# Kernel optimization log

Hardware: AMD Instinct MI355X
Metric: run time of the kernel (lower is better)

## Reference

```python
import jax, jax.numpy as jnp
import numpy as np

NB = 5  # frequency bands


def _ln(x, g, b, eps=1e-5):
    m = jnp.mean(x, axis=-1, keepdims=True)
    v = jnp.var(x, axis=-1, keepdims=True)
    return (x - m) / jnp.sqrt(v + eps) * g + b


def _graph_adj(x, adj_w, sw1, sb1, sw2, sb2, pos_factor, pos_enc):
    # x: [B, D, N] -> degree-normalized adjacency [B, N, N]
    d = x.shape[1]
    xt = jnp.swapaxes(x, 1, 2)  # [B, N, D]
    # concat-MLP first layer split: cat(xi, xj) @ W1 == xi @ W1[:d] + xj @ W1[d:]
    a = xt @ sw1[:d]
    bpart = xt @ sw1[d:]
    h = jax.nn.elu(a[:, :, None, :] + bpart[:, None, :, :] + sb1)  # [B, N, N, H]
    dyn = jax.nn.sigmoid(jnp.squeeze(h @ sw2, -1) + sb2)  # [B, N, N]
    static = jax.nn.softmax(adj_w, axis=-1)
    pos = jax.nn.softmax(pos_enc, axis=-1)
    comb = jax.nn.softmax(static + dyn + pos_factor * pos, axis=-1)
    deg = jnp.sum(comb, axis=-1)
    dis = (deg + 1e-8) ** -0.5
    return dis[:, :, None] * comb * dis[:, None, :]


def _gcn(x, adj, w, b):
    # x: [B, D, N], adj: [B, N, N] -> [B, D_out, N]
    xt = jnp.swapaxes(x, 1, 2)
    out = jnp.einsum('bij,bjd->bid', adj, xt) @ w + b
    return jnp.swapaxes(out, 1, 2)


def _mha(x, qkv_w, qkv_b, ow, ob, nh=4):
    B, S, D = x.shape
    dh = D // nh
    q, k, v = jnp.split(x @ qkv_w + qkv_b, 3, axis=-1)
    q = q.reshape(B, S, nh, dh)
    k = k.reshape(B, S, nh, dh)
    v = v.reshape(B, S, nh, dh)
    att = jax.nn.softmax(jnp.einsum('bihd,bjhd->bhij', q, k) / float(np.sqrt(dh)), axis=-1)
    o = jnp.einsum('bhij,bjhd->bihd', att, v).reshape(B, S, D)
    return o @ ow + ob


def setup_inputs():
    key = jax.random.key(0)
    B, D, N = 16, 256, 64
    ks = iter(jax.random.split(key, 40))

    def rn(shape, s=0.05):
        return jax.random.normal(next(ks), shape, dtype=jnp.float32) * s

    eyeN = jnp.eye(N, dtype=jnp.float32)
    return dict(
        feature=jax.random.normal(next(ks), (B, NB * D, 1, N), dtype=jnp.float32),
        l_adj_w=jnp.tile(eyeN[None], (NB, 1, 1)),
        l_sim_w1=rn((NB, 2 * D, D)), l_sim_b1=jnp.zeros((NB, D), jnp.float32),
        l_sim_w2=rn((NB, D, 1)), l_sim_b2=jnp.zeros((NB, 1), jnp.float32),
        l_pos_factor=jnp.full((NB,), 0.5, jnp.float32),
        l_pos_enc=jnp.tile(eyeN[None], (NB, 1, 1)),
        l_gcn_w=rn((NB, D, D)), l_gcn_b=jnp.zeros((NB, D), jnp.float32),
        g_adj_w=jnp.eye(NB, dtype=jnp.float32),
        g_sim_w1=rn((2 * D, D)), g_sim_b1=jnp.zeros((D,), jnp.float32),
        g_sim_w2=rn((D, 1)), g_sim_b2=jnp.zeros((1,), jnp.float32),
        g_pos_factor=jnp.float32(0.5),
        g_pos_enc=jnp.eye(NB, dtype=jnp.float32),
        g_gcn_w=rn((D, D)), g_gcn_b=jnp.zeros((D,), jnp.float32),
        qkv_w=rn((D, 3 * D)), qkv_b=jnp.zeros((3 * D,), jnp.float32),
        attn_ow=rn((D, D)), attn_ob=jnp.zeros((D,), jnp.float32),
        ln1_g=jnp.ones((D,), jnp.float32), ln1_b=jnp.zeros((D,), jnp.float32),
        ln2_g=jnp.ones((D,), jnp.float32), ln2_b=jnp.zeros((D,), jnp.float32),
        mlp_w1=rn((D, 4 * D)), mlp_b1=jnp.zeros((4 * D,), jnp.float32),
        mlp_w2=rn((4 * D, D)), mlp_b2=jnp.zeros((D,), jnp.float32),
        imp_w=rn((NB, N, 1)), imp_b=jnp.zeros((NB, 1), jnp.float32),
    )


def reference(feature, l_adj_w, l_sim_w1, l_sim_b1, l_sim_w2, l_sim_b2,
              l_pos_factor, l_pos_enc, l_gcn_w, l_gcn_b,
              g_adj_w, g_sim_w1, g_sim_b1, g_sim_w2, g_sim_b2,
              g_pos_factor, g_pos_enc, g_gcn_w, g_gcn_b,
              qkv_w, qkv_b, attn_ow, attn_ob,
              ln1_g, ln1_b, ln2_g, ln2_b,
              mlp_w1, mlp_b1, mlp_w2, mlp_b2,
              imp_w, imp_b):
    B = feature.shape[0]
    D = l_gcn_w.shape[-1]
    N = feature.shape[-1]
    # [B, 5*D, 1, N] -> [5, B, D, N] band-major
    x5 = jnp.moveaxis(feature.reshape(B, NB, D, N), 1, 0)
    # per-band local graphs + GCNs (vmapped over the 5 bands)
    local_adj = jax.vmap(_graph_adj)(x5, l_adj_w, l_sim_w1, l_sim_b1,
                                     l_sim_w2, l_sim_b2, l_pos_factor, l_pos_enc)
    local_out = jax.vmap(_gcn)(x5, local_adj, l_gcn_w, l_gcn_b)  # [5, B, D, N]
    scale_nodes = jnp.moveaxis(jnp.mean(local_out, axis=-1), 0, 1)  # [B, 5, D]
    # cross-band attention block (pre: MHA + residual + LN, then MLP + residual + LN)
    attn = _mha(scale_nodes, qkv_w, qkv_b, attn_ow, attn_ob)
    h1 = _ln(scale_nodes + attn, ln1_g, ln1_b)
    mlp = jax.nn.gelu(h1 @ mlp_w1 + mlp_b1, approximate=False) @ mlp_w2 + mlp_b2
    se = _ln(h1 + mlp, ln2_g, ln2_b)  # [B, 5, D]
    # global scale graph over the 5 band nodes
    xg = jnp.swapaxes(se, 1, 2)  # [B, D, 5]
    g_adj = _graph_adj(xg, g_adj_w, g_sim_w1, g_sim_b1, g_sim_w2, g_sim_b2,
                       g_pos_factor, g_pos_enc)
    g_out = jnp.swapaxes(_gcn(xg, g_adj, g_gcn_w, g_gcn_b), 1, 2)  # [B, 5, D]
    # modulate each local band feature by its global scale vector
    enh = local_out * jnp.moveaxis(g_out, 1, 0)[..., None]  # [5, B, D, N]
    # per-band importance projection over channels: [5, B, D, 1]
    out5 = jnp.einsum('kbdn,kno->kbdo', enh, imp_w) + imp_b[:, None, None, :]
    output = jnp.moveaxis(out5, 0, 1).reshape(B, NB * D, 1, 1)
    return output, g_adj, jnp.moveaxis(local_out, 0, 1)
```

## Files before the change

kernel.cpp:

```cpp
#include <hip/hip_runtime.h>
#include <hip/hip_bf16.h>

#define NBANDS 5
#define BATCH  16
#define DIM    256
#define NNODE  64
#define SEQ    5

typedef __hip_bfloat16 bf16;
typedef unsigned short ushort_t;
typedef __attribute__((ext_vector_type(8))) short short8;
typedef __attribute__((ext_vector_type(4))) float float4v;

#define MFMA __builtin_amdgcn_mfma_f32_16x16x32_bf16

__device__ __forceinline__ float bu2f(ushort_t u){
    bf16 h = *reinterpret_cast<bf16*>(&u);
    return __bfloat162float(h);
}
__device__ __forceinline__ ushort_t f2bu(float x){
    bf16 h = __float2bfloat16(x);
    return *reinterpret_cast<ushort_t*>(&h);
}
__device__ __forceinline__ float elu(float v){
    return (v > 0.f) ? v : (__expf(v) - 1.f);
}

__global__ void __launch_bounds__(256) k_head(
    const float* __restrict__ l_adj_w, const float* __restrict__ l_pos_enc,
    const float* __restrict__ l_pf,
    const float* __restrict__ g_adj_w, const float* __restrict__ g_pos_enc,
    const float* __restrict__ g_pf,
    float* __restrict__ sbase, float* __restrict__ gbase,
    const float* __restrict__ w1, const float* __restrict__ gw,
    ushort_t* __restrict__ w1bt, ushort_t* __restrict__ gwbt)
{
    int blk = blockIdx.x;
    int tid = threadIdx.x;
    __shared__ ushort_t tile[64][65];

    if (blk < 80) {
        int r = blk*4 + (tid>>6);
        int k = r >> 6, i = r & 63;
        int t = tid & 63;
        float aw = l_adj_w[(k*NNODE + i)*NNODE + t];
        float pe = l_pos_enc[(k*NNODE + i)*NNODE + t];
        float m1 = aw, m2 = pe;
        for (int o=32;o>0;o>>=1){ m1 = fmaxf(m1, __shfl_xor(m1,o,64)); m2 = fmaxf(m2, __shfl_xor(m2,o,64)); }
        float e1 = __expf(aw-m1), e2 = __expf(pe-m2);
        float s1=e1, s2=e2;
        for (int o=32;o>0;o>>=1){ s1 += __shfl_xor(s1,o,64); s2 += __shfl_xor(s2,o,64); }
        float pf = l_pf[k];
        sbase[(k*NNODE+i)*NNODE + t] = e1/s1 + pf*(e2/s2);
    } else if (blk == 80) {
        if (tid < NBANDS) {
            int i = tid;
            float r1[NBANDS], r2[NBANDS];
            float m1=-1e30f, m2=-1e30f;
            for (int j=0;j<NBANDS;j++){
                r1[j]=g_adj_w[i*NBANDS+j]; r2[j]=g_pos_enc[i*NBANDS+j];
                m1=fmaxf(m1,r1[j]); m2=fmaxf(m2,r2[j]);
            }
            float s1=0.f,s2=0.f;
            for (int j=0;j<NBANDS;j++){ r1[j]=__expf(r1[j]-m1); r2[j]=__expf(r2[j]-m2); s1+=r1[j]; s2+=r2[j]; }
            float pf = g_pf[0];
            for (int j=0;j<NBANDS;j++) gbase[i*NBANDS+j] = r1[j]/s1 + pf*(r2[j]/s2);
        }
    } else {
        int idx = blk - 81;
        int inst = idx >> 4;
        int t = idx & 15;
        int r0 = (t>>2)*64, c0 = (t&3)*64;
        const float* src; ushort_t* dst;
        if (inst < 10){
            int k = inst>>1, half = inst&1;
            src = w1  + ((size_t)k*512 + half*256)*256;
            dst = w1bt+ ((size_t)k*512 + half*256)*256;
        } else {
            int k = inst-10;
            src = gw  + (size_t)k*65536;
            dst = gwbt+ (size_t)k*65536;
        }
        int jj = tid & 63, i4 = tid >> 6;
        for (int p=0;p<16;p++){
            int i = p*4 + i4;
            tile[i][jj] = f2bu(src[(size_t)(r0+i)*256 + c0 + jj]);
        }
        __syncthreads();
        for (int p=0;p<16;p++){
            int i = p*4 + i4;
            dst[(size_t)(c0+i)*256 + r0 + jj] = tile[jj][i];
        }
    }
}

__global__ void __launch_bounds__(512) k_graph(
    const float* __restrict__ feat,
    const ushort_t* __restrict__ w1bt, const float* __restrict__ b1,
    const float* __restrict__ w2, const float* __restrict__ b2arr,
    const float* __restrict__ sbase,
    const ushort_t* __restrict__ gwbt, const float* __restrict__ gb,
    const float* __restrict__ imp_w,
    float* __restrict__ out_local,
    float* __restrict__ scalew4, float* __restrict__ impw4)
{
    int kb = blockIdx.x % 80;
    int iq = blockIdx.x / 80;
    int k  = kb >> 4;
    int b  = kb & 15;
    int i0 = iq << 4;
    int tid = threadIdx.x;
    int w = tid >> 6, lane = tid & 63, c16 = lane & 15, quad = lane >> 4;

    __shared__ ushort_t Ubuf[64*266 + 8];
    __shared__ ushort_t as[16][264];
    __shared__ ushort_t cs[16][72];
    __shared__ ushort_t ys[16][264];
    __shared__ float w2s[DIM];

    const float* src = feat + ((size_t)b*NBANDS + k)*DIM*NNODE;

    int il0 = w*2, il1 = w*2 + 1;
    float sb0 = sbase[(k*NNODE + i0 + il0)*NNODE + lane];
    float sb1 = sbase[(k*NNODE + i0 + il1)*NNODE + lane];
    float sbias2 = b2arr[k];

    if (tid < DIM) w2s[tid] = w2[k*DIM + tid];
    #pragma unroll
    for (int u = 0; u < 32; ++u){
        int idx = u*512 + tid;
        Ubuf[(idx & 63)*264 + (idx >> 6)] = f2bu(src[idx]);
    }
    __syncthreads();

    int col0 = w*32 + c16;
    int col1 = col0 + 16;

    const ushort_t* Ba = w1bt + (size_t)k*512*DIM;
    const ushort_t* Bb = Ba + 256*DIM;
    float4v z = {0.f,0.f,0.f,0.f};
    float4v aA0=z, aA1=z;
    float4v aB00=z,aB01=z,aB10=z,aB11=z,aB20=z,aB21=z,aB30=z,aB31=z;
    #pragma unroll
    for (int ks = 0; ks < 8; ++ks){
        int ko = ks*32 + quad*8;
        short8 fa = *reinterpret_cast<const short8*>(&Ubuf[(i0 + c16)*264 + ko]);
        short8 f0 = *reinterpret_cast<const short8*>(&Ubuf[( 0 + c16)*264 + ko]);
        short8 f1 = *reinterpret_cast<const short8*>(&Ubuf[(16 + c16)*264 + ko]);
        short8 f2 = *reinterpret_cast<const short8*>(&Ubuf[(32 + c16)*264 + ko]);
        short8 f3 = *reinterpret_cast<const short8*>(&Ubuf[(48 + c16)*264 + ko]);
        short8 wa0 = *reinterpret_cast<const short8*>(Ba + (size_t)col0*DIM + ko);
        short8 wa1 = *reinterpret_cast<const short8*>(Ba + (size_t)col1*DIM + ko);
        short8 wb0 = *reinterpret_cast<const short8*>(Bb + (size_t)col0*DIM + ko);
        short8 wb1 = *reinterpret_cast<const short8*>(Bb + (size_t)col1*DIM + ko);
        aA0  = MFMA(fa, wa0, aA0, 0,0,0);
        aA1  = MFMA(fa, wa1, aA1, 0,0,0);
        aB00 = MFMA(f0, wb0, aB00, 0,0,0);
        aB01 = MFMA(f0, wb1, aB01, 0,0,0);
        aB10 = MFMA(f1, wb0, aB10, 0,0,0);
        aB11 = MFMA(f1, wb1, aB11, 0,0,0);
        aB20 = MFMA(f2, wb0, aB20, 0,0,0);
        aB21 = MFMA(f2, wb1, aB21, 0,0,0);
        aB30 = MFMA(f3, wb0, aB30, 0,0,0);
        aB31 = MFMA(f3, wb1, aB31, 0,0,0);
    }
    __syncthreads();
    {
        float bias0 = b1[k*DIM + col0];
        float bias1 = b1[k*DIM + col1];
        int r0 = quad*4;
        #pragma unroll
        for (int r = 0; r < 4; ++r){
            as[r0 + r][col0] = f2bu(aA0[r] + bias0);
            as[r0 + r][col1] = f2bu(aA1[r] + bias1);
            Ubuf[( 0 + r0 + r)*266 + col0] = f2bu(aB00[r]);
            Ubuf[( 0 + r0 + r)*266 + col1] = f2bu(aB01[r]);
            Ubuf[(16 + r0 + r)*266 + col0] = f2bu(aB10[r]);
            Ubuf[(16 + r0 + r)*266 + col1] = f2bu(aB11[r]);
            Ubuf[(32 + r0 + r)*266 + col0] = f2bu(aB20[r]);
            Ubuf[(32 + r0 + r)*266 + col1] = f2bu(aB21[r]);
            Ubuf[(48 + r0 + r)*266 + col0] = f2bu(aB30[r]);
            Ubuf[(48 + r0 + r)*266 + col1] = f2bu(aB31[r]);
        }
    }
    __syncthreads();

    {
        const ushort_t* bd = Ubuf + 266*lane;
        const ushort_t* a0p = as[il0];
        const ushort_t* a1p = as[il1];
        float acc0 = 0.f, acc1 = 0.f;
        #pragma unroll 4
        for (int dd = 0; dd < 64; ++dd){
            unsigned int blo = *reinterpret_cast<const unsigned int*>(bd + dd*4);
            unsigned int bhi = *reinterpret_cast<const unsigned int*>(bd + dd*4 + 2);
            ushort4 a0 = *reinterpret_cast<const ushort4*>(a0p + dd*4);
            ushort4 a1 = *reinterpret_cast<const ushort4*>(a1p + dd*4);
            float4 wv  = *reinterpret_cast<const float4*>(&w2s[dd*4]);
            float bx = bu2f((ushort_t)(blo & 0xffffu));
            float by = bu2f((ushort_t)(blo >> 16));
            float bz = bu2f((ushort_t)(bhi & 0xffffu));
            float bq = bu2f((ushort_t)(bhi >> 16));
            acc0 += elu(bu2f(a0.x)+bx)*wv.x + elu(bu2f(a0.y)+by)*wv.y
                  + elu(bu2f(a0.z)+bz)*wv.z + elu(bu2f(a0.w)+bq)*wv.w;
            acc1 += elu(bu2f(a1.x)+bx)*wv.x + elu(bu2f(a1.y)+by)*wv.y
                  + elu(bu2f(a1.z)+bz)*wv.z + elu(bu2f(a1.w)+bq)*wv.w;
        }
        float sg0 = 1.f/(1.f + __expf(-(acc0 + sbias2)));
        float sg1 = 1.f/(1.f + __expf(-(acc1 + sbias2)));
        float val0 = sb0 + sg0;
        float val1 = sb1 + sg1;
        float m0 = val0, m1 = val1;
        for (int o=32;o>0;o>>=1){ m0 = fmaxf(m0, __shfl_xor(m0,o,64)); m1 = fmaxf(m1, __shfl_xor(m1,o,64)); }
        float e0 = __expf(val0 - m0), e1 = __expf(val1 - m1);
        float s0 = e0, s1 = e1;
        for (int o=32;o>0;o>>=1){ s0 += __shfl_xor(s0,o,64); s1 += __shfl_xor(s1,o,64); }
        cs[il0][lane] = f2bu(e0/s0);
        cs[il1][lane] = f2bu(e1/s1);
    }
    __syncthreads();

    float4v aY0 = z, aY1 = z;
    {
        #pragma unroll
        for (int ks = 0; ks < 2; ++ks){
            int ko = ks*32 + quad*8;
            short8 af = *reinterpret_cast<const short8*>(&cs[c16][ko]);
            const float* f0p = src + (size_t)col0*NNODE + ko;
            const float* f1p = src + (size_t)col1*NNODE + ko;
            float4 x0 = *reinterpret_cast<const float4*>(f0p);
            float4 x1 = *reinterpret_cast<const float4*>(f0p+4);
            float4 y0 = *reinterpret_cast<const float4*>(f1p);
            float4 y1 = *reinterpret_cast<const float4*>(f1p+4);
            short8 bf0, bf1;
            bf0[0]=(short)f2bu(x0.x); bf0[1]=(short)f2bu(x0.y); bf0[2]=(short)f2bu(x0.z); bf0[3]=(short)f2bu(x0.w);
            bf0[4]=(short)f2bu(x1.x); bf0[5]=(short)f2bu(x1.y); bf0[6]=(short)f2bu(x1.z); bf0[7]=(short)f2bu(x1.w);
            bf1[0]=(short)f2bu(y0.x); bf1[1]=(short)f2bu(y0.y); bf1[2]=(short)f2bu(y0.z); bf1[3]=(short)f2bu(y0.w);
            bf1[4]=(short)f2bu(y1.x); bf1[5]=(short)f2bu(y1.y); bf1[6]=(short)f2bu(y1.z); bf1[7]=(short)f2bu(y1.w);
            aY0 = MFMA(af, bf0, aY0, 0,0,0);
            aY1 = MFMA(af, bf1, aY1, 0,0,0);
        }
        #pragma unroll
        for (int r=0;r<4;++r){
            ys[quad*4 + r][col0] = f2bu(aY0[r]);
            ys[quad*4 + r][col1] = f2bu(aY1[r]);
        }
    }
    __syncthreads();

    {
        float4v aG0 = z, aG1 = z;
        const ushort_t* Bg = gwbt + (size_t)k*DIM*DIM;
        #pragma unroll
        for (int ks = 0; ks < 8; ++ks){
            int ko = ks*32 + quad*8;
            short8 af = *reinterpret_cast<const short8*>(&ys[c16][ko]);
            short8 g0 = *reinterpret_cast<const short8*>(Bg + (size_t)col0*DIM + ko);
            short8 g1 = *reinterpret_cast<const short8*>(Bg + (size_t)col1*DIM + ko);
            aG0 = MFMA(af, g0, aG0, 0,0,0);
            aG1 = MFMA(af, g1, aG1, 0,0,0);
        }
        int nb = i0 + quad*4;
        float iw0 = imp_w[k*NNODE + nb + 0];
        float iw1 = imp_w[k*NNODE + nb + 1];
        float iw2 = imp_w[k*NNODE + nb + 2];
        float iw3 = imp_w[k*NNODE + nb + 3];
        size_t obase = ((size_t)b*NBANDS + k)*DIM;

        float bias0 = gb[k*DIM + col0];
        float v0 = aG0[0]+bias0, v1 = aG0[1]+bias0, v2 = aG0[2]+bias0, v3 = aG0[3]+bias0;
        float4 vv = make_float4(v0,v1,v2,v3);
        *reinterpret_cast<float4*>(&out_local[(obase + col0)*NNODE + nb]) = vv;
        float s  = v0+v1+v2+v3;
        float di = v0*iw0 + v1*iw1 + v2*iw2 + v3*iw3;
        s  += __shfl_xor(s,16,64);  s  += __shfl_xor(s,32,64);
        di += __shfl_xor(di,16,64); di += __shfl_xor(di,32,64);
        if (quad == 0){
            size_t o = ((size_t)iq*80 + b*SEQ + k)*DIM + col0;
            scalew4[o] = s;
            impw4[o]   = di;
        }

        float bias1 = gb[k*DIM + col1];
        v0 = aG1[0]+bias1; v1 = aG1[1]+bias1; v2 = aG1[2]+bias1; v3 = aG1[3]+bias1;
        vv = make_float4(v0,v1,v2,v3);
        *reinterpret_cast<float4*>(&out_local[(obase + col1)*NNODE + nb]) = vv;
        s  = v0+v1+v2+v3;
        di = v0*iw0 + v1*iw1 + v2*iw2 + v3*iw3;
        s  += __shfl_xor(s,16,64);  s  += __shfl_xor(s,32,64);
        di += __shfl_xor(di,16,64); di += __shfl_xor(di,32,64);
        if (quad == 0){
            size_t o = ((size_t)iq*80 + b*SEQ + k)*DIM + col1;
            scalew4[o] = s;
            impw4[o]   = di;
        }
    }
}

__global__ void __launch_bounds__(256) k_qkv_gemv(const float* __restrict__ scalew4,
                        const float* __restrict__ w, const float* __restrict__ bias,
                        float* __restrict__ out)
{
    int row = blockIdx.x / 12;
    int n0 = (blockIdx.x % 12) * 64;
    int tid = threadIdx.x;
    int c = tid & 63, s = tid >> 6;
    __shared__ float xs[DIM];
    __shared__ float part[4][64];
    {
        size_t basei = (size_t)row*DIM + tid;
        xs[tid] = (scalew4[basei] + scalew4[20480 + basei]
                 + scalew4[40960 + basei] + scalew4[61440 + basei]) * (1.f/64.f);
    }
    __syncthreads();
    const float* wp = w + (size_t)(s*64)*768 + n0 + c;
    const float* xp = xs + s*64;
    float acc = 0.f;
    #pragma unroll 8
    for (int i = 0; i < 64; ++i) acc += xp[i] * wp[(size_t)i*768];
    part[s][c] = acc;
    __syncthreads();
    if (s == 0){
        out[(size_t)row*768 + n0 + c] = bias[n0+c] + part[0][c]+part[1][c]+part[2][c]+part[3][c];
    }
}

template<int COLS, int SLICES>
__global__ void __launch_bounds__(256) k_gemv(const float* __restrict__ x, const float* __restrict__ w,
                       const float* __restrict__ bias, float* __restrict__ out,
                       int K, int N, int act)
{
    int chunks = N / COLS;
    int row = blockIdx.x / chunks;
    int n0 = (blockIdx.x % chunks) * COLS;
    int c = threadIdx.x % COLS, s = threadIdx.x / COLS;
    __shared__ float xs[1024];
    __shared__ float part[SLICES][COLS];
    for (int i = threadIdx.x; i < K; i += 256) xs[i] = x[(size_t)row*K + i];
    __syncthreads();
    int klen = K / SLICES;
    const float* wp = w + (size_t)(s*klen)*N + n0 + c;
    const float* xp = xs + s*klen;
    float acc = 0.f;
    #pragma unroll 8
    for (int i = 0; i < klen; ++i) acc += xp[i] * wp[(size_t)i*N];
    part[s][c] = acc;
    __syncthreads();
    if (s == 0){
        float v = bias[n0+c];
        #pragma unroll
        for (int q=0;q<SLICES;q++) v += part[q][c];
        if (act) v = 0.5f*v*(1.f + erff(v*0.70710678118654752f));
        out[(size_t)row*N + n0 + c] = v;
    }
}

__global__ void __launch_bounds__(256) k_projattn(const float* __restrict__ qkvw,
                        const float* __restrict__ ow, const float* __restrict__ ob,
                        float* __restrict__ projw)
{
    int row = blockIdx.x / 4;
    int n0 = (blockIdx.x % 4) * 64;
    int b = row / SEQ, i = row % SEQ;
    int tid = threadIdx.x;
    int h = tid >> 6, l = tid & 63;
    __shared__ float xs[DIM];
    __shared__ float part[4][64];
    const float* base = qkvw + (size_t)b*SEQ*3*DIM;
    float qv = base[(size_t)i*3*DIM + h*64 + l];
    float pj[SEQ];
    #pragma unroll
    for (int j=0;j<SEQ;j++){
        float p = qv * base[(size_t)j*3*DIM + DIM + h*64 + l];
        for (int o=32;o>0;o>>=1) p += __shfl_xor(p,o,64);
        pj[j] = p * 0.125f;
    }
    float m = pj[0];
    #pragma unroll
    for (int j=1;j<SEQ;j++) m = fmaxf(m, pj[j]);
    float ssum = 0.f;
    #pragma unroll
    for (int j=0;j<SEQ;j++){ pj[j] = __expf(pj[j]-m); ssum += pj[j]; }
    float inv = 1.f/ssum;
    float o = 0.f;
    #pragma unroll
    for (int j=0;j<SEQ;j++) o += pj[j]*inv * base[(size_t)j*3*DIM + 2*DIM + h*64 + l];
    xs[tid] = o;
    __syncthreads();
    int c = tid & 63, s = tid >> 6;
    const float* wp = ow + (size_t)(s*64)*DIM + n0 + c;
    const float* xp = xs + s*64;
    float acc = 0.f;
    #pragma unroll 8
    for (int k=0;k<64;++k) acc += xp[k] * wp[(size_t)k*DIM];
    part[s][c] = acc;
    __syncthreads();
    if (s == 0){
        projw[(size_t)row*DIM + n0 + c] = ob[n0+c] + part[0][c]+part[1][c]+part[2][c]+part[3][c];
    }
}

__device__ __forceinline__ float block_ln(float v, int tid, float* red, float g, float bln)
{
    float s = v;
    for (int o=32;o>0;o>>=1) s += __shfl_xor(s,o,64);
    int wave = tid>>6, lane = tid&63;
    if (lane==0) red[wave] = s;
    __syncthreads();
    float mean = (red[0]+red[1]+red[2]+red[3]) * (1.f/DIM);
    float c = v - mean;
    float q = c*c;
    for (int o=32;o>0;o>>=1) q += __shfl_xor(q,o,64);
    __syncthreads();
    if (lane==0) red[wave] = q;
    __syncthreads();
    float var = (red[0]+red[1]+red[2]+red[3]) * (1.f/DIM);
    return c * rsqrtf(var + 1e-5f) * g + bln;
}

__global__ void __launch_bounds__(256) k_mlp1_ln(const float* __restrict__ projw,
                         const float* __restrict__ scalew4,
                         const float* __restrict__ ln1_g, const float* __restrict__ ln1_b,
                         const float* __restrict__ w1, const float* __restrict__ b1,
                         float* __restrict__ h1w, float* __restrict__ mhw)
{
    int row = blockIdx.x / 16;
    int n0 = (blockIdx.x % 16) * 64;
    int tid = threadIdx.x;
    __shared__ float xs[DIM];
    __shared__ float red[4];
    __shared__ float part[4][64];
    size_t basei = (size_t)row*DIM + tid;
    float sc = (scalew4[basei] + scalew4[20480 + basei]
              + scalew4[40960 + basei] + scalew4[61440 + basei]) * (1.f/64.f);
    float v = projw[basei] + sc;
    float h = block_ln(v, tid, red, ln1_g[tid], ln1_b[tid]);
    xs[tid] = h;
    if ((blockIdx.x % 16) == 0) h1w[basei] = h;
    __syncthreads();
    int c = tid & 63, s = tid >> 6;
    const float* wp = w1 + (size_t)(s*64)*1024 + n0 + c;
    const float* xp = xs + s*64;
    float acc = 0.f;
    #pragma unroll 8
    for (int i=0;i<64;++i) acc += xp[i] * wp[(size_t)i*1024];
    part[s][c] = acc;
    __syncthreads();
    if (s == 0){
        float o = b1[n0+c] + part[0][c] + part[1][c] + part[2][c] + part[3][c];
        o = 0.5f*o*(1.f + erff(o*0.70710678118654752f));
        mhw[(size_t)row*1024 + n0 + c] = o;
    }
}

__global__ void __launch_bounds__(256) k_gab_ln(const float* __restrict__ m2w,
                        const float* __restrict__ h1w,
                        const float* __restrict__ ln2_g, const float* __restrict__ ln2_b,
                        const float* __restrict__ gw1, const float* __restrict__ gb1,
                        float* __restrict__ sew, float* __restrict__ gaw, float* __restrict__ gbw)
{
    int row = blockIdx.x / 4;
    int n0 = (blockIdx.x % 4) * 64;
    int tid = threadIdx.x;
    __shared__ float xs[DIM];
    __shared__ float red[4];
    __shared__ float partA[4][64];
    __shared__ float partB[4][64];
    float v = m2w[(size_t)row*DIM + tid] + h1w[(size_t)row*DIM + tid];
    float h = block_ln(v, tid, red, ln2_g[tid], ln2_b[tid]);
    xs[tid] = h;
    if ((blockIdx.x % 4) == 0) sew[(size_t)row*DIM + tid] = h;
    __syncthreads();
    int c = tid & 63, s = tid >> 6;
    const float* wpA = gw1 + (size_t)(s*64)*DIM + n0 + c;
    const float* wpB = wpA + (size_t)DIM*DIM;
    const float* xp = xs + s*64;
    float aA = 0.f, aB = 0.f;
    #pragma unroll 8
    for (int i=0;i<64;++i){
        float xv = xp[i];
        aA += xv * wpA[(size_t)i*DIM];
        aB += xv * wpB[(size_t)i*DIM];
    }
    partA[s][c] = aA;
    partB[s][c] = aB;
    __syncthreads();
    if (s == 0){
        gaw[(size_t)row*DIM + n0 + c] = gb1[n0+c] + partA[0][c]+partA[1][c]+partA[2][c]+partA[3][c];
        gbw[(size_t)row*DIM + n0 + c] = partB[0][c]+partB[1][c]+partB[2][c]+partB[3][c];
    }
}

__global__ void __launch_bounds__(256) k_goutfin(const float* __restrict__ gaw,
                        const float* __restrict__ gbw,
                        const float* __restrict__ gw2, const float* __restrict__ gb2,
                        const float* __restrict__ gbase,
                        const float* __restrict__ sew,
                        const float* __restrict__ ggw, const float* __restrict__ ggb,
                        const float* __restrict__ impw4, const float* __restrict__ imp_b,
                        float* __restrict__ out0, float* __restrict__ out_gadj)
{
    int row = blockIdx.x / 4;
    int n0 = (blockIdx.x % 4) * 64;
    int b = row / SEQ, i = row % SEQ;
    int tid = threadIdx.x;
    int wave = tid >> 6, lane = tid & 63;
    __shared__ float dyn_s[SEQ];
    __shared__ float xs[DIM];
    __shared__ float part[4][64];
    for (int j = wave; j < SEQ; j += 4){
        const float* gar = gaw + (size_t)row*DIM;
        const float* gbr = gbw + ((size_t)b*SEQ + j)*DIM;
        float acc = 0.f;
        #pragma unroll
        for (int m=0;m<4;m++){
            int dd = lane + m*64;
            float v = gar[dd] + gbr[dd];
            acc += elu(v) * gw2[dd];
        }
        for (int o=32;o>0;o>>=1) acc += __shfl_xor(acc,o,64);
        if (lane==0) dyn_s[j] = acc;
    }
    __syncthreads();
    float gc[SEQ];
    {
        float sb2 = gb2[0];
        float m = -1e30f;
        #pragma unroll
        for (int j=0;j<SEQ;j++){
            float sg = 1.f/(1.f+__expf(-(dyn_s[j]+sb2)));
            gc[j] = gbase[i*SEQ+j] + sg;
            m = fmaxf(m, gc[j]);
        }
        float ssum=0.f;
        #pragma unroll
        for (int j=0;j<SEQ;j++){ gc[j]=__expf(gc[j]-m); ssum+=gc[j]; }
        float inv = 1.f/ssum;
        #pragma unroll
        for (int j=0;j<SEQ;j++) gc[j] *= inv;
    }
    if (n0 == 0 && tid < SEQ) out_gadj[((size_t)b*SEQ+i)*SEQ + tid] = gc[tid];
    float t = 0.f;
    #pragma unroll
    for (int j=0;j<SEQ;j++) t += gc[j]*sew[((size_t)b*SEQ + j)*DIM + tid];
    xs[tid] = t;
    __syncthreads();
    int c = tid & 63, s = tid >> 6;
    const float* wp = ggw + (size_t)(s*64)*DIM + n0 + c;
    const float* xp = xs + s*64;
    float acc = 0.f;
    #pragma unroll 8
    for (int k=0;k<64;++k) acc += xp[k] * wp[(size_t)k*DIM];
    part[s][c] = acc;
    __syncthreads();
    if (s == 0){
        float g = ggb[n0+c] + part[0][c]+part[1][c]+part[2][c]+part[3][c];
        size_t o = (size_t)row*DIM + n0 + c;
        float imps = impw4[o] + impw4[20480 + o] + impw4[40960 + o] + impw4[61440 + o];
        out0[o] = g * imps + imp_b[i];
    }
}

extern "C" void kernel_launch(void* const* d_in, const int* in_sizes, int n_in,
                              void* d_out, int out_size, void* d_ws, size_t ws_size,
                              hipStream_t stream)
{
    const float* feature      = (const float*)d_in[0];
    const float* l_adj_w      = (const float*)d_in[1];
    const float* l_sim_w1     = (const float*)d_in[2];
    const float* l_sim_b1     = (const float*)d_in[3];
    const float* l_sim_w2     = (const float*)d_in[4];
    const float* l_sim_b2     = (const float*)d_in[5];
    const float* l_pos_factor = (const float*)d_in[6];
    const float* l_pos_enc    = (const float*)d_in[7];
    const float* l_gcn_w      = (const float*)d_in[8];
    const float* l_gcn_b      = (const float*)d_in[9];
    const float* g_adj_w      = (const float*)d_in[10];
    const float* g_sim_w1     = (const float*)d_in[11];
    const float* g_sim_b1     = (const float*)d_in[12];
    const float* g_sim_w2     = (const float*)d_in[13];
    const float* g_sim_b2     = (const float*)d_in[14];
    const float* g_pos_factor = (const float*)d_in[15];
    const float* g_pos_enc    = (const float*)d_in[16];
    const float* g_gcn_w      = (const float*)d_in[17];
    const float* g_gcn_b      = (const float*)d_in[18];
    const float* qkv_w        = (const float*)d_in[19];
    const float* qkv_b        = (const float*)d_in[20];
    const float* attn_ow      = (const float*)d_in[21];
    const float* attn_ob      = (const float*)d_in[22];
    const float* ln1_g        = (const float*)d_in[23];
    const float* ln1_b        = (const float*)d_in[24];
    const float* ln2_g        = (const float*)d_in[25];
    const float* ln2_b        = (const float*)d_in[26];
    const float* mlp_w1       = (const float*)d_in[27];
    const float* mlp_b1       = (const float*)d_in[28];
    const float* mlp_w2       = (const float*)d_in[29];
    const float* mlp_b2       = (const float*)d_in[30];
    const float* imp_w        = (const float*)d_in[31];
    const float* imp_b        = (const float*)d_in[32];

    float* out0      = (float*)d_out;
    float* out_gadj  = out0 + (size_t)BATCH*NBANDS*DIM;
    float* out_local = out_gadj + (size_t)BATCH*NBANDS*NBANDS;

    ushort_t* w1bt = (ushort_t*)d_ws;
    ushort_t* gwbt = w1bt + (size_t)NBANDS*512*DIM;
    float* fp = (float*)(gwbt + (size_t)NBANDS*DIM*DIM);
    float* sbase   = fp; fp += NBANDS*NNODE*NNODE;
    float* gbase   = fp; fp += 32;
    float* scalew4 = fp; fp += 4*BATCH*SEQ*DIM;
    float* impw4   = fp; fp += 4*BATCH*SEQ*DIM;
    float* qkvw    = fp; fp += BATCH*SEQ*3*DIM;
    float* projw   = fp; fp += BATCH*SEQ*DIM;
    float* h1w     = fp; fp += BATCH*SEQ*DIM;
    float* mhw     = fp; fp += BATCH*SEQ*4*DIM;
    float* m2w     = fp; fp += BATCH*SEQ*DIM;
    float* sew     = fp; fp += BATCH*SEQ*DIM;
    float* gaw     = fp; fp += BATCH*SEQ*DIM;
    float* gbw     = fp; fp += BATCH*SEQ*DIM;

    const int ROWS = BATCH*SEQ;

    k_head<<<321, 256, 0, stream>>>(l_adj_w, l_pos_enc, l_pos_factor,
                                    g_adj_w, g_pos_enc, g_pos_factor,
                                    sbase, gbase,
                                    l_sim_w1, l_gcn_w, w1bt, gwbt);
    k_graph<<<NBANDS*BATCH*4, 512, 0, stream>>>(feature, w1bt, l_sim_b1,
                                    l_sim_w2, l_sim_b2, sbase,
                                    gwbt, l_gcn_b, imp_w,
                                    out_local, scalew4, impw4);
    k_qkv_gemv<<<ROWS*12, 256, 0, stream>>>(scalew4, qkv_w, qkv_b, qkvw);
    k_projattn<<<ROWS*4, 256, 0, stream>>>(qkvw, attn_ow, attn_ob, projw);
    k_mlp1_ln<<<ROWS*16, 256, 0, stream>>>(projw, scalew4, ln1_g, ln1_b, mlp_w1, mlp_b1, h1w, mhw);
    k_gemv<32,8><<<ROWS*8, 256, 0, stream>>>(mhw, mlp_w2, mlp_b2, m2w, 1024, 256, 0);
    k_gab_ln<<<ROWS*4, 256, 0, stream>>>(m2w, h1w, ln2_g, ln2_b, g_sim_w1, g_sim_b1, sew, gaw, gbw);
    k_goutfin<<<ROWS*4, 256, 0, stream>>>(gaw, gbw, g_sim_w2, g_sim_b2, gbase,
                                          sew, g_gcn_w, g_gcn_b, impw4, imp_b,
                                          out0, out_gadj);
}
```

Before: 215.8 us.

## Merge six tail kernels into one cooperative kernel with grid syncs

The six small GEMV/attention/LayerNorm tail kernels become a single cooperative kernel whose stages are separated by grid.sync() and use grid-stride loops over the original block tasks. The goal is to remove five kernel launch gaps and tail drains between tiny dependent stages. k_graph also changes: the feature transpose now packs 8 bf16 values per 16-byte LDS store, the w2 staging buffer is dropped in favour of direct global reads, and the ys buffer reuses Ubuf to cut shared-memory use. The risks are grid-sync overhead, and a launch failure if 960 blocks cannot all be co-resident for the cooperative launch.

After: 795.0 us. +268.3%, slower.

```diff
diff --git a/kernel.cpp b/kernel.cpp
--- a/kernel.cpp
+++ b/kernel.cpp
@@ -1,5 +1,8 @@
 #include <hip/hip_runtime.h>
 #include <hip/hip_bf16.h>
+#include <hip/hip_cooperative_groups.h>
+
+namespace cg = cooperative_groups;
 
 #define NBANDS 5
 #define BATCH  16
@@ -24,6 +27,9 @@
 }
 __device__ __forceinline__ float elu(float v){
     return (v > 0.f) ? v : (__expf(v) - 1.f);
+}
+__device__ __forceinline__ float sum4(const float* __restrict__ p, size_t i){
+    return p[i] + p[20480 + i] + p[40960 + i] + p[61440 + i];
 }
 
 __global__ void __launch_bounds__(256) k_head(
@@ -112,11 +118,10 @@
     int tid = threadIdx.x;
     int w = tid >> 6, lane = tid & 63, c16 = lane & 15, quad = lane >> 4;
 
-    __shared__ ushort_t Ubuf[64*266 + 8];
-    __shared__ ushort_t as[16][264];
-    __shared__ ushort_t cs[16][72];
-    __shared__ ushort_t ys[16][264];
-    __shared__ float w2s[DIM];
+    __shared__ __align__(16) ushort_t Ubuf[64*266 + 8];
+    __shared__ __align__(16) ushort_t as[16][260];
+    __shared__ __align__(16) ushort_t cs[16][72];
+    ushort_t* ys = Ubuf;
 
     const float* src = feat + ((size_t)b*NBANDS + k)*DIM*NNODE;
 
@@ -125,11 +130,15 @@
     float sb1 = sbase[(k*NNODE + i0 + il1)*NNODE + lane];
     float sbias2 = b2arr[k];
 
-    if (tid < DIM) w2s[tid] = w2[k*DIM + tid];
     #pragma unroll
-    for (int u = 0; u < 32; ++u){
-        int idx = u*512 + tid;
-        Ubuf[(idx & 63)*264 + (idx >> 6)] = f2bu(src[idx]);
+    for (int u = 0; u < 4; ++u){
+        int t = u*512 + tid;
+        int n = t & 63;
+        int d0 = (t >> 6) * 8;
+        short8 pk;
+        #pragma unroll
+        for (int i = 0; i < 8; ++i) pk[i] = (short)f2bu(src[(size_t)(d0+i)*NNODE + n]);
+        *reinterpret_cast<short8*>(&Ubuf[(size_t)n*264 + d0]) = pk;
     }
     __syncthreads();
 
@@ -187,8 +196,9 @@
 
     {
         const ushort_t* bd = Ubuf + 266*lane;
-        const ushort_t* a0p = as[il0];
-        const ushort_t* a1p = as[il1];
+        const ushort_t* a0p = &as[il0][0];
+        const ushort_t* a1p = &as[il1][0];
+        const float* w2p = w2 + k*DIM;
         float acc0 = 0.f, acc1 = 0.f;
         #pragma unroll 4
         for (int dd = 0; dd < 64; ++dd){
@@ -196,7 +206,7 @@
             unsigned int bhi = *reinterpret_cast<const unsigned int*>(bd + dd*4 + 2);
             ushort4 a0 = *reinterpret_cast<const ushort4*>(a0p + dd*4);
             ushort4 a1 = *reinterpret_cast<const ushort4*>(a1p + dd*4);
-            float4 wv  = *reinterpret_cast<const float4*>(&w2s[dd*4]);
+            float4 wv  = *reinterpret_cast<const float4*>(w2p + dd*4);
             float bx = bu2f((ushort_t)(blo & 0xffffu));
             float by = bu2f((ushort_t)(blo >> 16));
             float bz = bu2f((ushort_t)(bhi & 0xffffu));
@@ -220,8 +230,8 @@
     }
     __syncthreads();
 
-    float4v aY0 = z, aY1 = z;
     {
+        float4v aY0 = z, aY1 = z;
         #pragma unroll
         for (int ks = 0; ks < 2; ++ks){
             int ko = ks*32 + quad*8;
@@ -242,8 +252,8 @@
         }
         #pragma unroll
         for (int r=0;r<4;++r){
-            ys[quad*4 + r][col0] = f2bu(aY0[r]);
-            ys[quad*4 + r][col1] = f2bu(aY1[r]);
+            ys[(quad*4 + r)*264 + col0] = f2bu(aY0[r]);
+            ys[(quad*4 + r)*264 + col1] = f2bu(aY1[r]);
         }
     }
     __syncthreads();
@@ -254,7 +264,7 @@
         #pragma unroll
         for (int ks = 0; ks < 8; ++ks){
             int ko = ks*32 + quad*8;
-            short8 af = *reinterpret_cast<const short8*>(&ys[c16][ko]);
+            short8 af = *reinterpret_cast<const short8*>(&ys[c16*264 + ko]);
             short8 g0 = *reinterpret_cast<const short8*>(Bg + (size_t)col0*DIM + ko);
             short8 g1 = *reinterpret_cast<const short8*>(Bg + (size_t)col1*DIM + ko);
             aG0 = MFMA(af, g0, aG0, 0,0,0);
@@ -269,134 +279,31 @@
 
         float bias0 = gb[k*DIM + col0];
         float v0 = aG0[0]+bias0, v1 = aG0[1]+bias0, v2 = aG0[2]+bias0, v3 = aG0[3]+bias0;
-        float4 vv = make_float4(v0,v1,v2,v3);
-        *reinterpret_cast<float4*>(&out_local[(obase + col0)*NNODE + nb]) = vv;
+        *reinterpret_cast<float4*>(&out_local[(obase + col0)*NNODE + nb]) =
+            make_float4(v0,v1,v2,v3);
         float s  = v0+v1+v2+v3;
         float di = v0*iw0 + v1*iw1 + v2*iw2 + v3*iw3;
         s  += __shfl_xor(s,16,64);  s  += __shfl_xor(s,32,64);
         di += __shfl_xor(di,16,64); di += __shfl_xor(di,32,64);
         if (quad == 0){
-            size_t o = ((size_t)iq*80 + b*SEQ + k)*DIM + col0;
+            size_t o = (size_t)iq*20480 + ((size_t)b*SEQ + k)*DIM + col0;
             scalew4[o] = s;
             impw4[o]   = di;
         }
 
         float bias1 = gb[k*DIM + col1];
         v0 = aG1[0]+bias1; v1 = aG1[1]+bias1; v2 = aG1[2]+bias1; v3 = aG1[3]+bias1;
-        vv = make_float4(v0,v1,v2,v3);
-        *reinterpret_cast<float4*>(&out_local[(obase + col1)*NNODE + nb]) = vv;
+        *reinterpret_cast<float4*>(&out_local[(obase + col1)*NNODE + nb]) =
+            make_float4(v0,v1,v2,v3);
         s  = v0+v1+v2+v3;
         di = v0*iw0 + v1*iw1 + v2*iw2 + v3*iw3;
         s  += __shfl_xor(s,16,64);  s  += __shfl_xor(s,32,64);
         di += __shfl_xor(di,16,64); di += __shfl_xor(di,32,64);
         if (quad == 0){
-            size_t o = ((size_t)iq*80 + b*SEQ + k)*DIM + col1;
+            size_t o = (size_t)iq*20480 + ((size_t)b*SEQ + k)*DIM + col1;
             scalew4[o] = s;
             impw4[o]   = di;
         }
-    }
-}
-
-__global__ void __launch_bounds__(256) k_qkv_gemv(const float* __restrict__ scalew4,
-                        const float* __restrict__ w, const float* __restrict__ bias,
-                        float* __restrict__ out)
-{
-    int row = blockIdx.x / 12;
-    int n0 = (blockIdx.x % 12) * 64;
-    int tid = threadIdx.x;
-    int c = tid & 63, s = tid >> 6;
-    __shared__ float xs[DIM];
-    __shared__ float part[4][64];
-    {
-        size_t basei = (size_t)row*DIM + tid;
-        xs[tid] = (scalew4[basei] + scalew4[20480 + basei]
-                 + scalew4[40960 + basei] + scalew4[61440 + basei]) * (1.f/64.f);
-    }
-    __syncthreads();
-    const float* wp = w + (size_t)(s*64)*768 + n0 + c;
-    const float* xp = xs + s*64;
-    float acc = 0.f;
-    #pragma unroll 8
-    for (int i = 0; i < 64; ++i) acc += xp[i] * wp[(size_t)i*768];
-    part[s][c] = acc;
-    __syncthreads();
-    if (s == 0){
-        out[(size_t)row*768 + n0 + c] = bias[n0+c] + part[0][c]+part[1][c]+part[2][c]+part[3][c];
-    }
-}
-
-template<int COLS, int SLICES>
-__global__ void __launch_bounds__(256) k_gemv(const float* __restrict__ x, const float* __restrict__ w,
-                       const float* __restrict__ bias, float* __restrict__ out,
-                       int K, int N, int act)
-{
-    int chunks = N / COLS;
-    int row = blockIdx.x / chunks;
-    int n0 = (blockIdx.x % chunks) * COLS;
-    int c = threadIdx.x % COLS, s = threadIdx.x / COLS;
-    __shared__ float xs[1024];
-    __shared__ float part[SLICES][COLS];
-    for (int i = threadIdx.x; i < K; i += 256) xs[i] = x[(size_t)row*K + i];
-    __syncthreads();
-    int klen = K / SLICES;
-    const float* wp = w + (size_t)(s*klen)*N + n0 + c;
-    const float* xp = xs + s*klen;
-    float acc = 0.f;
-    #pragma unroll 8
-    for (int i = 0; i < klen; ++i) acc += xp[i] * wp[(size_t)i*N];
-    part[s][c] = acc;
-    __syncthreads();
-    if (s == 0){
-        float v = bias[n0+c];
-        #pragma unroll
-        for (int q=0;q<SLICES;q++) v += part[q][c];
-        if (act) v = 0.5f*v*(1.f + erff(v*0.70710678118654752f));
-        out[(size_t)row*N + n0 + c] = v;
-    }
-}
-
-__global__ void __launch_bounds__(256) k_projattn(const float* __restrict__ qkvw,
-                        const float* __restrict__ ow, const float* __restrict__ ob,
-                        float* __restrict__ projw)
-{
-    int row = blockIdx.x / 4;
-    int n0 = (blockIdx.x % 4) * 64;
-    int b = row / SEQ, i = row % SEQ;
-    int tid = threadIdx.x;
-    int h = tid >> 6, l = tid & 63;
-    __shared__ float xs[DIM];
-    __shared__ float part[4][64];
-    const float* base = qkvw + (size_t)b*SEQ*3*DIM;
-    float qv = base[(size_t)i*3*DIM + h*64 + l];
-    float pj[SEQ];
-    #pragma unroll
-    for (int j=0;j<SEQ;j++){
-        float p = qv * base[(size_t)j*3*DIM + DIM + h*64 + l];
-        for (int o=32;o>0;o>>=1) p += __shfl_xor(p,o,64);
-        pj[j] = p * 0.125f;
-    }
-    float m = pj[0];
-    #pragma unroll
-    for (int j=1;j<SEQ;j++) m = fmaxf(m, pj[j]);
-    float ssum = 0.f;
-    #pragma unroll
-    for (int j=0;j<SEQ;j++){ pj[j] = __expf(pj[j]-m); ssum += pj[j]; }
-    float inv = 1.f/ssum;
-    float o = 0.f;
-    #pragma unroll
-    for (int j=0;j<SEQ;j++) o += pj[j]*inv * base[(size_t)j*3*DIM + 2*DIM + h*64 + l];
-    xs[tid] = o;
-    __syncthreads();
-    int c = tid & 63, s = tid >> 6;
-    const float* wp = ow + (size_t)(s*64)*DIM + n0 + c;
-    const float* xp = xs + s*64;
-    float acc = 0.f;
-    #pragma unroll 8
-    for (int k=0;k<64;++k) acc += xp[k] * wp[(size_t)k*DIM];
-    part[s][c] = acc;
-    __syncthreads();
-    if (s == 0){
-        projw[(size_t)row*DIM + n0 + c] = ob[n0+c] + part[0][c]+part[1][c]+part[2][c]+part[3][c];
     }
 }
 
@@ -418,146 +325,220 @@
     return c * rsqrtf(var + 1e-5f) * g + bln;
 }
 
-__global__ void __launch_bounds__(256) k_mlp1_ln(const float* __restrict__ projw,
-                         const float* __restrict__ scalew4,
-                         const float* __restrict__ ln1_g, const float* __restrict__ ln1_b,
-                         const float* __restrict__ w1, const float* __restrict__ b1,
-                         float* __restrict__ h1w, float* __restrict__ mhw)
+struct TailArgs {
+    const float *scalew4, *impw4;
+    const float *qkv_w, *qkv_b, *attn_ow, *attn_ob;
+    const float *ln1_g, *ln1_b, *mlp_w1, *mlp_b1, *mlp_w2, *mlp_b2;
+    const float *ln2_g, *ln2_b, *gw1, *gb1, *gw2, *gb2, *gbase;
+    const float *ggw, *ggb, *imp_b;
+    float *qkvw, *projw, *h1w, *mhw, *m2w, *sew, *gaw, *gbw;
+    float *out0, *out_gadj;
+};
+
+__global__ void __launch_bounds__(256, 4) k_tail_coop(TailArgs A)
 {
-    int row = blockIdx.x / 16;
-    int n0 = (blockIdx.x % 16) * 64;
-    int tid = threadIdx.x;
-    __shared__ float xs[DIM];
-    __shared__ float red[4];
-    __shared__ float part[4][64];
-    size_t basei = (size_t)row*DIM + tid;
-    float sc = (scalew4[basei] + scalew4[20480 + basei]
-              + scalew4[40960 + basei] + scalew4[61440 + basei]) * (1.f/64.f);
-    float v = projw[basei] + sc;
-    float h = block_ln(v, tid, red, ln1_g[tid], ln1_b[tid]);
-    xs[tid] = h;
-    if ((blockIdx.x % 16) == 0) h1w[basei] = h;
-    __syncthreads();
-    int c = tid & 63, s = tid >> 6;
-    const float* wp = w1 + (size_t)(s*64)*1024 + n0 + c;
-    const float* xp = xs + s*64;
-    float acc = 0.f;
-    #pragma unroll 8
-    for (int i=0;i<64;++i) acc += xp[i] * wp[(size_t)i*1024];
-    part[s][c] = acc;
-    __syncthreads();
-    if (s == 0){
-        float o = b1[n0+c] + part[0][c] + part[1][c] + part[2][c] + part[3][c];
-        o = 0.5f*o*(1.f + erff(o*0.70710678118654752f));
-        mhw[(size_t)row*1024 + n0 + c] = o;
-    }
-}
-
-__global__ void __launch_bounds__(256) k_gab_ln(const float* __restrict__ m2w,
-                        const float* __restrict__ h1w,
-                        const float* __restrict__ ln2_g, const float* __restrict__ ln2_b,
-                        const float* __restrict__ gw1, const float* __restrict__ gb1,
-                        float* __restrict__ sew, float* __restrict__ gaw, float* __restrict__ gbw)
-{
-    int row = blockIdx.x / 4;
-    int n0 = (blockIdx.x % 4) * 64;
-    int tid = threadIdx.x;
-    __shared__ float xs[DIM];
-    __shared__ float red[4];
-    __shared__ float partA[4][64];
-    __shared__ float partB[4][64];
-    float v = m2w[(size_t)row*DIM + tid] + h1w[(size_t)row*DIM + tid];
-    float h = block_ln(v, tid, red, ln2_g[tid], ln2_b[tid]);
-    xs[tid] = h;
-    if ((blockIdx.x % 4) == 0) sew[(size_t)row*DIM + tid] = h;
-    __syncthreads();
-    int c = tid & 63, s = tid >> 6;
-    const float* wpA = gw1 + (size_t)(s*64)*DIM + n0 + c;
-    const float* wpB = wpA + (size_t)DIM*DIM;
-    const float* xp = xs + s*64;
-    float aA = 0.f, aB = 0.f;
-    #pragma unroll 8
-    for (int i=0;i<64;++i){
-        float xv = xp[i];
-        aA += xv * wpA[(size_t)i*DIM];
-        aB += xv * wpB[(size_t)i*DIM];
-    }
-    partA[s][c] = aA;
-    partB[s][c] = aB;
-    __syncthreads();
-    if (s == 0){
-        gaw[(size_t)row*DIM + n0 + c] = gb1[n0+c] + partA[0][c]+partA[1][c]+partA[2][c]+partA[3][c];
-        gbw[(size_t)row*DIM + n0 + c] = partB[0][c]+partB[1][c]+partB[2][c]+partB[3][c];
-    }
-}
-
-__global__ void __launch_bounds__(256) k_goutfin(const float* __restrict__ gaw,
-                        const float* __restrict__ gbw,
-                        const float* __restrict__ gw2, const float* __restrict__ gb2,
-                        const float* __restrict__ gbase,
-                        const float* __restrict__ sew,
-                        const float* __restrict__ ggw, const float* __restrict__ ggb,
-                        const float* __restrict__ impw4, const float* __restrict__ imp_b,
-                        float* __restrict__ out0, float* __restrict__ out_gadj)
-{
-    int row = blockIdx.x / 4;
-    int n0 = (blockIdx.x % 4) * 64;
-    int b = row / SEQ, i = row % SEQ;
+    cg::grid_group grid = cg::this_grid();
+    const int NBLK = gridDim.x;
     int tid = threadIdx.x;
     int wave = tid >> 6, lane = tid & 63;
-    __shared__ float dyn_s[SEQ];
-    __shared__ float xs[DIM];
-    __shared__ float part[4][64];
-    for (int j = wave; j < SEQ; j += 4){
-        const float* gar = gaw + (size_t)row*DIM;
-        const float* gbr = gbw + ((size_t)b*SEQ + j)*DIM;
+    __shared__ float xs[1024];
+    __shared__ float red[4];
+    __shared__ float part8[8][64];
+    __shared__ float dyn_s[8];
+
+    for (int t = blockIdx.x; t < 960; t += NBLK){
+        int row = t / 12, n0 = (t % 12) * 64;
+        int c = tid & 63, s = tid >> 6;
+        xs[tid] = sum4(A.scalew4, (size_t)row*DIM + tid) * (1.f/64.f);
+        __syncthreads();
+        const float* wp = A.qkv_w + (size_t)(s*64)*768 + n0 + c;
+        const float* xp = xs + s*64;
         float acc = 0.f;
-        #pragma unroll
-        for (int m=0;m<4;m++){
-            int dd = lane + m*64;
-            float v = gar[dd] + gbr[dd];
-            acc += elu(v) * gw2[dd];
-        }
-        for (int o=32;o>0;o>>=1) acc += __shfl_xor(acc,o,64);
-        if (lane==0) dyn_s[j] = acc;
-    }
-    __syncthreads();
-    float gc[SEQ];
-    {
-        float sb2 = gb2[0];
-        float m = -1e30f;
+        #pragma unroll 8
+        for (int i = 0; i < 64; ++i) acc += xp[i] * wp[(size_t)i*768];
+        part8[s][c] = acc;
+        __syncthreads();
+        if (s == 0)
+            A.qkvw[(size_t)row*768 + n0 + c] = A.qkv_b[n0+c]
+                + part8[0][c]+part8[1][c]+part8[2][c]+part8[3][c];
+        __syncthreads();
+    }
+    grid.sync();
+
+    for (int t = blockIdx.x; t < 320; t += NBLK){
+        int row = t / 4, n0 = (t % 4) * 64;
+        int b = row / SEQ, i = row % SEQ;
+        int h = wave, l = lane;
+        const float* base = A.qkvw + (size_t)b*SEQ*3*DIM;
+        float qv = base[(size_t)i*3*DIM + h*64 + l];
+        float pj[SEQ];
         #pragma unroll
         for (int j=0;j<SEQ;j++){
-            float sg = 1.f/(1.f+__expf(-(dyn_s[j]+sb2)));
-            gc[j] = gbase[i*SEQ+j] + sg;
-            m = fmaxf(m, gc[j]);
-        }
-        float ssum=0.f;
-        #pragma unroll
-        for (int j=0;j<SEQ;j++){ gc[j]=__expf(gc[j]-m); ssum+=gc[j]; }
+            float p = qv * base[(size_t)j*3*DIM + DIM + h*64 + l];
+            for (int o=32;o>0;o>>=1) p += __shfl_xor(p,o,64);
+            pj[j] = p * 0.125f;
+        }
+        float m = pj[0];
+        #pragma unroll
+        for (int j=1;j<SEQ;j++) m = fmaxf(m, pj[j]);
+        float ssum = 0.f;
+        #pragma unroll
+        for (int j=0;j<SEQ;j++){ pj[j] = __expf(pj[j]-m); ssum += pj[j]; }
         float inv = 1.f/ssum;
-        #pragma unroll
-        for (int j=0;j<SEQ;j++) gc[j] *= inv;
-    }
-    if (n0 == 0 && tid < SEQ) out_gadj[((size_t)b*SEQ+i)*SEQ + tid] = gc[tid];
-    float t = 0.f;
-    #pragma unroll
-    for (int j=0;j<SEQ;j++) t += gc[j]*sew[((size_t)b*SEQ + j)*DIM + tid];
-    xs[tid] = t;
-    __syncthreads();
-    int c = tid & 63, s = tid >> 6;
-    const float* wp = ggw + (size_t)(s*64)*DIM + n0 + c;
-    const float* xp = xs + s*64;
-    float acc = 0.f;
-    #pragma unroll 8
-    for (int k=0;k<64;++k) acc += xp[k] * wp[(size_t)k*DIM];
-    part[s][c] = acc;
-    __syncthreads();
-    if (s == 0){
-        float g = ggb[n0+c] + part[0][c]+part[1][c]+part[2][c]+part[3][c];
-        size_t o = (size_t)row*DIM + n0 + c;
-        float imps = impw4[o] + impw4[20480 + o] + impw4[40960 + o] + impw4[61440 + o];
-        out0[o] = g * imps + imp_b[i];
+        float o = 0.f;
+        #pragma unroll
+        for (int j=0;j<SEQ;j++) o += pj[j]*inv * base[(size_t)j*3*DIM + 2*DIM + h*64 + l];
+        xs[tid] = o;
+        __syncthreads();
+        int c = tid & 63, s = tid >> 6;
+        const float* wp = A.attn_ow + (size_t)(s*64)*DIM + n0 + c;
+        const float* xp = xs + s*64;
+        float acc = 0.f;
+        #pragma unroll 8
+        for (int kk=0;kk<64;++kk) acc += xp[kk] * wp[(size_t)kk*DIM];
+        part8[s][c] = acc;
+        __syncthreads();
+        if (s == 0)
+            A.projw[(size_t)row*DIM + n0 + c] = A.attn_ob[n0+c]
+                + part8[0][c]+part8[1][c]+part8[2][c]+part8[3][c];
+        __syncthreads();
+    }
+    grid.sync();
+
+    for (int t = blockIdx.x; t < 1280; t += NBLK){
+        int row = t / 16, n0 = (t % 16) * 64;
+        size_t basei = (size_t)row*DIM + tid;
+        float sc = sum4(A.scalew4, basei) * (1.f/64.f);
+        float v = A.projw[basei] + sc;
+        float hh = block_ln(v, tid, red, A.ln1_g[tid], A.ln1_b[tid]);
+        xs[tid] = hh;
+        if ((t % 16) == 0) A.h1w[basei] = hh;
+        __syncthreads();
+        int c = tid & 63, s = tid >> 6;
+        const float* wp = A.mlp_w1 + (size_t)(s*64)*1024 + n0 + c;
+        const float* xp = xs + s*64;
+        float acc = 0.f;
+        #pragma unroll 8
+        for (int i=0;i<64;++i) acc += xp[i] * wp[(size_t)i*1024];
+        part8[s][c] = acc;
+        __syncthreads();
+        if (s == 0){
+            float o = A.mlp_b1[n0+c] + part8[0][c]+part8[1][c]+part8[2][c]+part8[3][c];
+            o = 0.5f*o*(1.f + erff(o*0.70710678118654752f));
+            A.mhw[(size_t)row*1024 + n0 + c] = o;
+        }
+        __syncthreads();
+    }
+    grid.sync();
+
+    for (int t = blockIdx.x; t < 640; t += NBLK){
+        int row = t / 8, n0 = (t % 8) * 32;
+        for (int i = tid; i < 1024; i += 256) xs[i] = A.mhw[(size_t)row*1024 + i];
+        __syncthreads();
+        int c = tid & 31, s = tid >> 5;
+        const float* wp = A.mlp_w2 + (size_t)(s*128)*DIM + n0 + c;
+        const float* xp = xs + s*128;
+        float acc = 0.f;
+        #pragma unroll 8
+        for (int i = 0; i < 128; ++i) acc += xp[i] * wp[(size_t)i*DIM];
+        (&part8[0][0])[s*32 + c] = acc;
+        __syncthreads();
+        if (s == 0){
+            float v = A.mlp_b2[n0+c];
+            #pragma unroll
+            for (int q=0;q<8;q++) v += (&part8[0][0])[q*32 + c];
+            A.m2w[(size_t)row*DIM + n0 + c] = v;
+        }
+        __syncthreads();
+    }
+    grid.sync();
+
+    for (int t = blockIdx.x; t < 320; t += NBLK){
+        int row = t / 4, n0 = (t % 4) * 64;
+        float v = A.m2w[(size_t)row*DIM + tid] + A.h1w[(size_t)row*DIM + tid];
+        float hh = block_ln(v, tid, red, A.ln2_g[tid], A.ln2_b[tid]);
+        xs[tid] = hh;
+        if ((t % 4) == 0) A.sew[(size_t)row*DIM + tid] = hh;
+        __syncthreads();
+        int c = tid & 63, s = tid >> 6;
+        const float* wpA = A.gw1 + (size_t)(s*64)*DIM + n0 + c;
+        const float* wpB = wpA + (size_t)DIM*DIM;
+        const float* xp = xs + s*64;
+        float aA = 0.f, aB = 0.f;
+        #pragma unroll 8
+        for (int i=0;i<64;++i){
+            float xv = xp[i];
+            aA += xv * wpA[(size_t)i*DIM];
+            aB += xv * wpB[(size_t)i*DIM];
+        }
+        part8[s][c] = aA;
+        part8[4+s][c] = aB;
+        __syncthreads();
+        if (s == 0){
+            A.gaw[(size_t)row*DIM + n0 + c] = A.gb1[n0+c]
+                + part8[0][c]+part8[1][c]+part8[2][c]+part8[3][c];
+            A.gbw[(size_t)row*DIM + n0 + c] =
+                  part8[4][c]+part8[5][c]+part8[6][c]+part8[7][c];
+        }
+        __syncthreads();
+    }
+    grid.sync();
+
+    for (int t = blockIdx.x; t < 320; t += NBLK){
+        int row = t / 4, n0 = (t % 4) * 64;
+        int b = row / SEQ, i = row % SEQ;
+        for (int j = wave; j < SEQ; j += 4){
+            const float* gar = A.gaw + (size_t)row*DIM;
+            const float* gbr = A.gbw + ((size_t)b*SEQ + j)*DIM;
+            float acc = 0.f;
+            #pragma unroll
+            for (int m=0;m<4;m++){
+                int dd = lane + m*64;
+                float v = gar[dd] + gbr[dd];
+                acc += elu(v) * A.gw2[dd];
+            }
+            for (int o=32;o>0;o>>=1) acc += __shfl_xor(acc,o,64);
+            if (lane==0) dyn_s[j] = acc;
+        }
+        __syncthreads();
+        float gc[SEQ];
+        {
+            float sb2 = A.gb2[0];
+            float m = -1e30f;
+            #pragma unroll
+            for (int j=0;j<SEQ;j++){
+                float sg = 1.f/(1.f+__expf(-(dyn_s[j]+sb2)));
+                gc[j] = A.gbase[i*SEQ+j] + sg;
+                m = fmaxf(m, gc[j]);
+            }
+            float ssum=0.f;
+            #pragma unroll
+            for (int j=0;j<SEQ;j++){ gc[j]=__expf(gc[j]-m); ssum+=gc[j]; }
+            float inv = 1.f/ssum;
+            #pragma unroll
+            for (int j=0;j<SEQ;j++) gc[j] *= inv;
+        }
+        if (n0 == 0 && tid < SEQ) A.out_gadj[((size_t)b*SEQ+i)*SEQ + tid] = gc[tid];
+        float tv = 0.f;
+        #pragma unroll
+        for (int j=0;j<SEQ;j++) tv += gc[j]*A.sew[((size_t)b*SEQ + j)*DIM + tid];
+        xs[tid] = tv;
+        __syncthreads();
+        int c = tid & 63, s = tid >> 6;
+        const float* wp = A.ggw + (size_t)(s*64)*DIM + n0 + c;
+        const float* xp = xs + s*64;
+        float acc = 0.f;
+        #pragma unroll 8
+        for (int kk=0;kk<64;++kk) acc += xp[kk] * wp[(size_t)kk*DIM];
+        part8[s][c] = acc;
+        __syncthreads();
+        if (s == 0){
+            float g = A.ggb[n0+c] + part8[0][c]+part8[1][c]+part8[2][c]+part8[3][c];
+            size_t o = (size_t)row*DIM + n0 + c;
+            float imps = sum4(A.impw4, o);
+            A.out0[o] = g * imps + A.imp_b[i];
+        }
+        __syncthreads();
     }
 }
 
@@ -619,8 +600,6 @@
     float* gaw     = fp; fp += BATCH*SEQ*DIM;
     float* gbw     = fp; fp += BATCH*SEQ*DIM;
 
-    const int ROWS = BATCH*SEQ;
-
     k_head<<<321, 256, 0, stream>>>(l_adj_w, l_pos_enc, l_pos_factor,
                                     g_adj_w, g_pos_enc, g_pos_factor,
                                     sbase, gbase,
@@ -629,12 +608,25 @@
                                     l_sim_w2, l_sim_b2, sbase,
                                     gwbt, l_gcn_b, imp_w,
                                     out_local, scalew4, impw4);
-    k_qkv_gemv<<<ROWS*12, 256, 0, stream>>>(scalew4, qkv_w, qkv_b, qkvw);
-    k_projattn<<<ROWS*4, 256, 0, stream>>>(qkvw, attn_ow, attn_ob, projw);
-    k_mlp1_ln<<<ROWS*16, 256, 0, stream>>>(projw, scalew4, ln1_g, ln1_b, mlp_w1, mlp_b1, h1w, mhw);
-    k_gemv<32,8><<<ROWS*8, 256, 0, stream>>>(mhw, mlp_w2, mlp_b2, m2w, 1024, 256, 0);
-    k_gab_ln<<<ROWS*4, 256, 0, stream>>>(m2w, h1w, ln2_g, ln2_b, g_sim_w1, g_sim_b1, sew, gaw, gbw);
-    k_goutfin<<<ROWS*4, 256, 0, stream>>>(gaw, gbw, g_sim_w2, g_sim_b2, gbase,
-                                          sew, g_gcn_w, g_gcn_b, impw4, imp_b,
-                                          out0, out_gadj);
-}
+
+    TailArgs ta;
+    ta.scalew4 = scalew4; ta.impw4 = impw4;
+    ta.qkv_w = qkv_w;     ta.qkv_b = qkv_b;
+    ta.attn_ow = attn_ow; ta.attn_ob = attn_ob;
+    ta.ln1_g = ln1_g;     ta.ln1_b = ln1_b;
+    ta.mlp_w1 = mlp_w1;   ta.mlp_b1 = mlp_b1;
+    ta.mlp_w2 = mlp_w2;   ta.mlp_b2 = mlp_b2;
+    ta.ln2_g = ln2_g;     ta.ln2_b = ln2_b;
+    ta.gw1 = g_sim_w1;    ta.gb1 = g_sim_b1;
+    ta.gw2 = g_sim_w2;    ta.gb2 = g_sim_b2;
+    ta.gbase = gbase;
+    ta.ggw = g_gcn_w;     ta.ggb = g_gcn_b;
+    ta.imp_b = imp_b;
+    ta.qkvw = qkvw; ta.projw = projw; ta.h1w = h1w; ta.mhw = mhw;
+    ta.m2w = m2w;   ta.sew = sew;     ta.gaw = gaw; ta.gbw = gbw;
+    ta.out0 = out0; ta.out_gadj = out_gadj;
+
+    void* params[] = { &ta };
+    hipLaunchCooperativeKernel((void*)k_tail_coop, dim3(960), dim3(256),
+                               params, 0, stream);
+}
```
